# Optimization experiments

Measured on AMD Instinct MI355X. Metric: run time of the kernel, lower is better.

## Reference

```python
import jax, jax.numpy as jnp
import numpy as np

N_NODES = 100000


def gcn_layer(x, W, b, src, dst, n):
    # PyG GCNConv: h = x @ W; add self loops; norm = d^-1/2[src]*d^-1/2[dst];
    # out = scatter_add(norm * h[src] -> dst) + b
    h = x @ W  # [N, F_out]
    # append self loops
    loop = jnp.arange(n, dtype=src.dtype)
    s = jnp.concatenate([src, loop])
    d = jnp.concatenate([dst, loop])
    deg = jax.ops.segment_sum(jnp.ones_like(d, dtype=h.dtype), d, num_segments=n)
    dinv = jnp.where(deg > 0, jax.lax.rsqrt(deg), 0.0)
    norm = dinv[s] * dinv[d]  # [E+N]
    msg = h[s] * norm[:, None]  # gather + scale
    out = jax.ops.segment_sum(msg, d, num_segments=n)  # scatter-add
    return out + b


def setup_inputs() -> dict:
    key = jax.random.key(0)
    k1, k2, k3, k4 = jax.random.split(key, 4)
    din, dh = 64, 64
    x = jax.random.normal(k1, (N_NODES, din), dtype=jnp.float32)
    edge_index = jax.random.randint(k2, (2, 1600000), 0, N_NODES, dtype=jnp.int64)
    s1 = 1.0 / np.sqrt(din)
    s2 = 1.0 / np.sqrt(dh)
    W1 = jax.random.uniform(k3, (din, dh), dtype=jnp.float32, minval=-s1, maxval=s1)
    W2 = jax.random.uniform(k4, (dh, dh), dtype=jnp.float32, minval=-s2, maxval=s2)
    b1 = jnp.zeros((dh,), dtype=jnp.float32)
    b2 = jnp.zeros((dh,), dtype=jnp.float32)
    return {"x": x, "edge_index": edge_index, "W1": W1, "b1": b1, "W2": W2, "b2": b2}


def reference(x, edge_index, W1, b1, W2, b2):
    src, dst = edge_index[0], edge_index[1]
    n = x.shape[0]
    h = jax.nn.relu(gcn_layer(x, W1, b1, src, dst, n))
    h = jax.nn.relu(gcn_layer(h, W2, b2, src, dst, n))
    return h
```

## Files before the change

### kernel.cpp

```cpp
#include <hip/hip_runtime.h>
#include <hip/hip_bf16.h>

using bf16s = __hip_bfloat16;
typedef __bf16 bf16x8 __attribute__((ext_vector_type(8)));
typedef float f32x4 __attribute__((ext_vector_type(4)));

constexpr int MS_TILE = 4096;
constexpr int BSH = 8;
constexpr int BN = 256;
constexpr int NBUCK = 512;
constexpr int SLAB_CAP = 5120;
constexpr int CSR_CAP = 6912;

__device__ inline float uasf(unsigned u) { return __uint_as_float(u); }

__device__ inline unsigned pk2(float x, float y) {
    unsigned ux = __float_as_uint(x), uy = __float_as_uint(y);
    ux = (ux + 0x7fffu + ((ux >> 16) & 1u)) >> 16;
    uy = (uy + 0x7fffu + ((uy >> 16) & 1u)) & 0xffff0000u;
    return (ux & 0xffffu) | uy;
}

__global__ __launch_bounds__(256) void multisplit(const int* __restrict__ src,
                                                  const int* __restrict__ dst,
                                                  int* __restrict__ gcur,
                                                  int* __restrict__ part, int E) {
    __shared__ int cnt[NBUCK];
    __shared__ int off[NBUCK];
    __shared__ int gbase[NBUCK];
    __shared__ int img[MS_TILE];
    __shared__ int tgt[MS_TILE];
    int tid = threadIdx.x;
    int tbase = blockIdx.x * MS_TILE;
    int m = min(MS_TILE, E - tbase);
    for (int i = tid; i < NBUCK; i += 256) cnt[i] = 0;
    __syncthreads();
    int pk[16], bk[16], rk[16];
    int nloc = 0;
    int j0 = tid * 16;
    if (j0 + 16 <= m) {
#pragma unroll
        for (int h = 0; h < 4; h++) {
            int4 s4 = *(const int4*)(src + tbase + j0 + 4 * h);
            int4 d4 = *(const int4*)(dst + tbase + j0 + 4 * h);
            int ss[4] = {s4.x, s4.y, s4.z, s4.w};
            int dd[4] = {d4.x, d4.y, d4.z, d4.w};
#pragma unroll
            for (int k = 0; k < 4; k++) {
                int i = 4 * h + k;
                int b = dd[k] >> BSH;
                pk[i] = (ss[k] << BSH) | (dd[k] & (BN - 1));
                bk[i] = b;
                rk[i] = atomicAdd(&cnt[b], 1);
            }
        }
        nloc = 16;
    } else {
        for (int j = j0; j < m; j++) {
            int s = src[tbase + j], d = dst[tbase + j];
            int b = d >> BSH;
            pk[nloc] = (s << BSH) | (d & (BN - 1));
            bk[nloc] = b;
            rk[nloc] = atomicAdd(&cnt[b], 1);
            nloc++;
        }
    }
    __syncthreads();
    if (tid < 64) {
        int base = tid * 8;
        int vals[8];
        int s0 = 0;
#pragma unroll
        for (int j = 0; j < 8; j++) { vals[j] = cnt[base + j]; s0 += vals[j]; }
        int sc = s0;
#pragma unroll
        for (int o = 1; o < 64; o <<= 1) {
            int u = __shfl_up(sc, o);
            if (tid >= o) sc += u;
        }
        int ex = sc - s0;
#pragma unroll
        for (int j = 0; j < 8; j++) { off[base + j] = ex; ex += vals[j]; }
    }
    __syncthreads();
    for (int b = tid; b < NBUCK; b += 256) {
        int c = cnt[b];
        if (c) {
            int st = atomicAdd(&gcur[b], c);
            if (st > SLAB_CAP - c) st = SLAB_CAP - c;
            gbase[b] = b * SLAB_CAP + st;
        }
    }
    __syncthreads();
    for (int i = 0; i < nloc; i++) {
        int p = off[bk[i]] + rk[i];
        img[p] = pk[i];
        tgt[p] = gbase[bk[i]] + rk[i];
    }
    __syncthreads();
    for (int j = tid; j < m; j += 256) part[tgt[j]] = img[j];
}

__global__ __launch_bounds__(256) void bucket_place(const int* __restrict__ gcur,
                                                    const int* __restrict__ part,
                                                    int2* __restrict__ rinfo,
                                                    int* __restrict__ csr,
                                                    float* __restrict__ dinv, int n) {
    __shared__ int cnt[BN];
    __shared__ int cur[BN];
    __shared__ int wtot[4];
    __shared__ int img[CSR_CAP];
    int b = blockIdx.x;
    int tid = threadIdx.x;
    int node0 = b << BSH;
    int m = min(gcur[b], SLAB_CAP);
    const int* slab = part + b * SLAB_CAP;
    cnt[tid] = 0;
    __syncthreads();
    for (int j = tid; j < m; j += 256) atomicAdd(&cnt[slab[j] & (BN - 1)], 1);
    __syncthreads();
    int deg = cnt[tid];
    int pdeg = (deg + 7) & ~7;
    int lane = tid & 63, wv = tid >> 6;
    int sc = pdeg;
#pragma unroll
    for (int o = 1; o < 64; o <<= 1) {
        int u = __shfl_up(sc, o);
        if (lane >= o) sc += u;
    }
    if (lane == 63) wtot[wv] = sc;
    __syncthreads();
    int wbase = 0;
#pragma unroll
    for (int k = 0; k < 4; k++) wbase += (k < wv) ? wtot[k] : 0;
    int mpad = wtot[0] + wtot[1] + wtot[2] + wtot[3];
    int ex = sc - pdeg + wbase;
    cur[tid] = ex;
    int node = node0 + tid;
    if (node < n) {
        rinfo[node] = make_int2(b * CSR_CAP + ex, pdeg);
        dinv[node] = rsqrtf((float)(deg + 1));
    }
    int sent = n << 5;
    for (int j = ex + deg; j < ex + pdeg; j++) img[j] = sent;
    __syncthreads();
    for (int j = tid; j < m; j += 256) {
        int pkv = slab[j];
        int p = atomicAdd(&cur[pkv & (BN - 1)], 1);
        img[p] = (pkv >> BSH) << 5;
    }
    __syncthreads();
    int* dp = csr + b * CSR_CAP;
    for (int j = tid; j < mpad; j += 256) dp[j] = img[j];
}

template <bool AF32>
__global__ __launch_bounds__(256) void gemm64(const void* __restrict__ A_,
                                              const float* __restrict__ W,
                                              const float* __restrict__ dinv,
                                              bf16s* __restrict__ out, int nrows) {
    int lane = threadIdx.x & 63;
    int wid = (blockIdx.x * blockDim.x + threadIdx.x) >> 6;
    int nwaves = (gridDim.x * blockDim.x) >> 6;
    int r = lane & 15;
    int q = lane >> 4;
    int kb = q * 8;

    if (wid == 0) out[(size_t)nrows * 64 + lane] = __float2bfloat16(0.f);

    bf16x8 bfrag[4][2];
#pragma unroll
    for (int t = 0; t < 4; t++) {
#pragma unroll
        for (int h = 0; h < 2; h++) {
            bf16x8 bb;
            int ncol = t * 16 + r;
            int k0 = h * 32 + kb;
#pragma unroll
            for (int j = 0; j < 8; j++) bb[j] = (__bf16)W[(k0 + j) * 64 + ncol];
            bfrag[t][h] = bb;
        }
    }

    int ntiles = nrows >> 4;
    for (int tile = wid; tile < ntiles; tile += nwaves) {
        bf16x8 a0, a1;
        if (AF32) {
            const float* ap = (const float*)A_ + (size_t)(tile * 16 + r) * 64 + kb;
            f32x4 v0 = *reinterpret_cast<const f32x4*>(ap);
            f32x4 v1 = *reinterpret_cast<const f32x4*>(ap + 4);
            f32x4 v2 = *reinterpret_cast<const f32x4*>(ap + 32);
            f32x4 v3 = *reinterpret_cast<const f32x4*>(ap + 36);
#pragma unroll
            for (int j = 0; j < 4; j++) {
                a0[j] = (__bf16)v0[j]; a0[4 + j] = (__bf16)v1[j];
                a1[j] = (__bf16)v2[j]; a1[4 + j] = (__bf16)v3[j];
            }
        } else {
            const __bf16* ap = (const __bf16*)A_ + (size_t)(tile * 16 + r) * 64 + kb;
            a0 = *reinterpret_cast<const bf16x8*>(ap);
            a1 = *reinterpret_cast<const bf16x8*>(ap + 32);
        }
        f32x4 c[4];
#pragma unroll
        for (int t = 0; t < 4; t++) {
            f32x4 acc = {0.f, 0.f, 0.f, 0.f};
            acc = __builtin_amdgcn_mfma_f32_16x16x32_bf16(a0, bfrag[t][0], acc, 0, 0, 0);
            acc = __builtin_amdgcn_mfma_f32_16x16x32_bf16(a1, bfrag[t][1], acc, 0, 0, 0);
            c[t] = acc;
        }
        float dr[4];
#pragma unroll
        for (int g = 0; g < 4; g++) dr[g] = dinv[tile * 16 + q * 4 + g];
#pragma unroll
        for (int t = 0; t < 4; t++) {
#pragma unroll
            for (int g = 0; g < 4; g++) {
                int row = tile * 16 + q * 4 + g;
                out[(size_t)row * 64 + t * 16 + r] = __float2bfloat16(c[t][g] * dr[g]);
            }
        }
    }
}

template <bool OUTF32>
__global__ __launch_bounds__(256) void aggregate(const unsigned* __restrict__ t32,
                                                 const float* __restrict__ dinv,
                                                 const int2* __restrict__ rinfo,
                                                 const int* __restrict__ csr,
                                                 const float* __restrict__ bias,
                                                 void* __restrict__ out_, int n) {
    int gid = blockIdx.x * blockDim.x + threadIdx.x;
    int qw = gid >> 4;
    int v0 = qw * 2, v1 = v0 + 1;
    if (v0 >= n) return;
    bool has1 = v1 < n;
    int c = gid & 15;
    int2 r0 = rinfo[v0];
    int2 r1 = has1 ? rinfo[v1] : make_int2(0, 0);
    uint2 s0 = *(const uint2*)(t32 + (size_t)v0 * 32 + 2 * c);
    uint2 s1 = has1 ? *(const uint2*)(t32 + (size_t)v1 * 32 + 2 * c) : make_uint2(0, 0);
    float a00 = uasf(s0.x << 16), a01 = uasf(s0.x & 0xffff0000u);
    float a02 = uasf(s0.y << 16), a03 = uasf(s0.y & 0xffff0000u);
    float a10 = uasf(s1.x << 16), a11 = uasf(s1.x & 0xffff0000u);
    float a12 = uasf(s1.y << 16), a13 = uasf(s1.y & 0xffff0000u);
    const int* cp0 = csr + r0.x;
    const int* cp1 = csr + r1.x;
    int j0 = 0, j1 = 0;
    while (j0 < r0.y || j1 < r1.y) {
        bool g0 = j0 < r0.y, g1 = j1 < r1.y;
        int idx0[8], idx1[8];
        uint2 ga[8], gb[8];
        if (g0) {
            int4 e0 = *(const int4*)(cp0 + j0);
            int4 e1 = *(const int4*)(cp0 + j0 + 4);
            idx0[0]=e0.x; idx0[1]=e0.y; idx0[2]=e0.z; idx0[3]=e0.w;
            idx0[4]=e1.x; idx0[5]=e1.y; idx0[6]=e1.z; idx0[7]=e1.w;
#pragma unroll
            for (int k = 0; k < 8; k++)
                ga[k] = *(const uint2*)(t32 + (size_t)idx0[k] + 2 * c);
        }
        if (g1) {
            int4 e0 = *(const int4*)(cp1 + j1);
            int4 e1 = *(const int4*)(cp1 + j1 + 4);
            idx1[0]=e0.x; idx1[1]=e0.y; idx1[2]=e0.z; idx1[3]=e0.w;
            idx1[4]=e1.x; idx1[5]=e1.y; idx1[6]=e1.z; idx1[7]=e1.w;
#pragma unroll
            for (int k = 0; k < 8; k++)
                gb[k] = *(const uint2*)(t32 + (size_t)idx1[k] + 2 * c);
        }
        if (g0) {
#pragma unroll
            for (int k = 0; k < 8; k++) {
                a00 += uasf(ga[k].x << 16);
                a01 += uasf(ga[k].x & 0xffff0000u);
                a02 += uasf(ga[k].y << 16);
                a03 += uasf(ga[k].y & 0xffff0000u);
            }
            j0 += 8;
        }
        if (g1) {
#pragma unroll
            for (int k = 0; k < 8; k++) {
                a10 += uasf(gb[k].x << 16);
                a11 += uasf(gb[k].x & 0xffff0000u);
                a12 += uasf(gb[k].y << 16);
                a13 += uasf(gb[k].y & 0xffff0000u);
            }
            j1 += 8;
        }
    }
    f32x4 bb = ((const f32x4*)bias)[c];
    {
        float dv = dinv[v0];
        float o0 = fmaxf(fmaf(dv, a00, bb[0]), 0.f);
        float o1 = fmaxf(fmaf(dv, a01, bb[1]), 0.f);
        float o2 = fmaxf(fmaf(dv, a02, bb[2]), 0.f);
        float o3 = fmaxf(fmaf(dv, a03, bb[3]), 0.f);
        if (OUTF32) {
            f32x4 o4 = {o0, o1, o2, o3};
            ((f32x4*)out_)[(size_t)v0 * 16 + c] = o4;
        } else {
            uint2 ou; ou.x = pk2(o0, o1); ou.y = pk2(o2, o3);
            ((uint2*)out_)[(size_t)v0 * 16 + c] = ou;
        }
    }
    if (has1) {
        float dv = dinv[v1];
        float o0 = fmaxf(fmaf(dv, a10, bb[0]), 0.f);
        float o1 = fmaxf(fmaf(dv, a11, bb[1]), 0.f);
        float o2 = fmaxf(fmaf(dv, a12, bb[2]), 0.f);
        float o3 = fmaxf(fmaf(dv, a13, bb[3]), 0.f);
        if (OUTF32) {
            f32x4 o4 = {o0, o1, o2, o3};
            ((f32x4*)out_)[(size_t)v1 * 16 + c] = o4;
        } else {
            uint2 ou; ou.x = pk2(o0, o1); ou.y = pk2(o2, o3);
            ((uint2*)out_)[(size_t)v1 * 16 + c] = ou;
        }
    }
}

extern "C" void kernel_launch(void* const* d_in, const int* in_sizes, int n_in,
                              void* d_out, int out_size, void* d_ws, size_t ws_size,
                              hipStream_t stream) {
    const float* x  = (const float*)d_in[0];
    const int*   ei = (const int*)d_in[1];
    const float* W1 = (const float*)d_in[2];
    const float* b1 = (const float*)d_in[3];
    const float* W2 = (const float*)d_in[4];
    const float* b2 = (const float*)d_in[5];
    float* out = (float*)d_out;

    int n = in_sizes[0] / 64;
    int E = in_sizes[1] / 2;
    const int* src = ei;
    const int* dst = ei + E;
    int nbuck = (n + BN - 1) >> BSH;

    char* w = (char*)d_ws;
    auto alloc = [&](size_t bytes) -> void* {
        void* p = (void*)w;
        w += (bytes + 255) & ~(size_t)255;
        return p;
    };
    int*   gcur   = (int*)alloc(NBUCK * 4);
    int2*  rinfo  = (int2*)alloc((size_t)n * 8);
    int*   csr    = (int*)alloc((size_t)nbuck * CSR_CAP * 4);
    float* dinv   = (float*)alloc((size_t)n * 4);
    size_t slab_bytes = (size_t)nbuck * SLAB_CAP * 4;
    size_t tbuf_bytes = (size_t)(n + 16) * 64 * 2;
    char*  ovl    = (char*)alloc(slab_bytes > tbuf_bytes ? slab_bytes : tbuf_bytes);
    int*   part   = (int*)ovl;
    bf16s* tbuf   = (bf16s*)ovl;
    bf16s* h1     = (bf16s*)alloc((size_t)(n + 16) * 64 * 2);

    hipMemsetAsync(gcur, 0, NBUCK * 4, stream);

    int ntiles = (E + MS_TILE - 1) / MS_TILE;
    multisplit<<<ntiles, 256, 0, stream>>>(src, dst, gcur, part, E);
    bucket_place<<<nbuck, 256, 0, stream>>>(gcur, part, rinfo, csr, dinv, n);

    int agrid = (n * 8 + 255) / 256;
    gemm64<true><<<256, 256, 0, stream>>>(x, W1, dinv, tbuf, n);
    aggregate<false><<<agrid, 256, 0, stream>>>((const unsigned*)tbuf, dinv, rinfo, csr, b1, h1, n);
    gemm64<false><<<256, 256, 0, stream>>>(h1, W2, dinv, tbuf, n);
    aggregate<true><<<agrid, 256, 0, stream>>>((const unsigned*)tbuf, dinv, rinfo, csr, b2, out, n);
}
```

Before: 201.0 us.

## Scatter partition and CSR writes directly to global, drop LDS staging

The multisplit kernel no longer stages edges in shared memory with a bucket prefix scan before writing coalesced runs. Each thread now writes its packed edges straight to their global slab slot, and the tile shrinks to 2048 edges (8 per thread). The bucket_place kernel likewise writes sentinels and CSR entries straight to global instead of building an LDS image and copying it out. This removes a scan, several barriers and a large LDS footprint, which may raise occupancy, at the cost of scattered, uncoalesced global writes and more global atomics on the bucket counters.

```diff
diff --git a/kernel.cpp b/kernel.cpp
--- a/kernel.cpp
+++ b/kernel.cpp
@@ -5,7 +5,7 @@
 typedef __bf16 bf16x8 __attribute__((ext_vector_type(8)));
 typedef float f32x4 __attribute__((ext_vector_type(4)));
 
-constexpr int MS_TILE = 4096;
+constexpr int MS_TILE = 2048;
 constexpr int BSH = 8;
 constexpr int BN = 256;
 constexpr int NBUCK = 512;
@@ -26,35 +26,30 @@
                                                   int* __restrict__ gcur,
                                                   int* __restrict__ part, int E) {
     __shared__ int cnt[NBUCK];
-    __shared__ int off[NBUCK];
     __shared__ int gbase[NBUCK];
-    __shared__ int img[MS_TILE];
-    __shared__ int tgt[MS_TILE];
     int tid = threadIdx.x;
     int tbase = blockIdx.x * MS_TILE;
     int m = min(MS_TILE, E - tbase);
     for (int i = tid; i < NBUCK; i += 256) cnt[i] = 0;
     __syncthreads();
-    int pk[16], bk[16], rk[16];
+    int pk[8], bk[8], rk[8];
     int nloc = 0;
-    int j0 = tid * 16;
-    if (j0 + 16 <= m) {
-#pragma unroll
-        for (int h = 0; h < 4; h++) {
-            int4 s4 = *(const int4*)(src + tbase + j0 + 4 * h);
-            int4 d4 = *(const int4*)(dst + tbase + j0 + 4 * h);
-            int ss[4] = {s4.x, s4.y, s4.z, s4.w};
-            int dd[4] = {d4.x, d4.y, d4.z, d4.w};
-#pragma unroll
-            for (int k = 0; k < 4; k++) {
-                int i = 4 * h + k;
-                int b = dd[k] >> BSH;
-                pk[i] = (ss[k] << BSH) | (dd[k] & (BN - 1));
-                bk[i] = b;
-                rk[i] = atomicAdd(&cnt[b], 1);
-            }
-        }
-        nloc = 16;
+    int j0 = tid * 8;
+    if (j0 + 8 <= m) {
+        int4 s0 = *(const int4*)(src + tbase + j0);
+        int4 s1 = *(const int4*)(src + tbase + j0 + 4);
+        int4 d0 = *(const int4*)(dst + tbase + j0);
+        int4 d1 = *(const int4*)(dst + tbase + j0 + 4);
+        int ss[8] = {s0.x, s0.y, s0.z, s0.w, s1.x, s1.y, s1.z, s1.w};
+        int dd[8] = {d0.x, d0.y, d0.z, d0.w, d1.x, d1.y, d1.z, d1.w};
+#pragma unroll
+        for (int k = 0; k < 8; k++) {
+            int b = dd[k] >> BSH;
+            pk[k] = (ss[k] << BSH) | (dd[k] & (BN - 1));
+            bk[k] = b;
+            rk[k] = atomicAdd(&cnt[b], 1);
+        }
+        nloc = 8;
     } else {
         for (int j = j0; j < m; j++) {
             int s = src[tbase + j], d = dst[tbase + j];
@@ -66,23 +61,6 @@
         }
     }
     __syncthreads();
-    if (tid < 64) {
-        int base = tid * 8;
-        int vals[8];
-        int s0 = 0;
-#pragma unroll
-        for (int j = 0; j < 8; j++) { vals[j] = cnt[base + j]; s0 += vals[j]; }
-        int sc = s0;
-#pragma unroll
-        for (int o = 1; o < 64; o <<= 1) {
-            int u = __shfl_up(sc, o);
-            if (tid >= o) sc += u;
-        }
-        int ex = sc - s0;
-#pragma unroll
-        for (int j = 0; j < 8; j++) { off[base + j] = ex; ex += vals[j]; }
-    }
-    __syncthreads();
     for (int b = tid; b < NBUCK; b += 256) {
         int c = cnt[b];
         if (c) {
@@ -92,13 +70,9 @@
         }
     }
     __syncthreads();
-    for (int i = 0; i < nloc; i++) {
-        int p = off[bk[i]] + rk[i];
-        img[p] = pk[i];
-        tgt[p] = gbase[bk[i]] + rk[i];
-    }
-    __syncthreads();
-    for (int j = tid; j < m; j += 256) part[tgt[j]] = img[j];
+#pragma unroll
+    for (int i = 0; i < 8; i++)
+        if (i < nloc) part[gbase[bk[i]] + rk[i]] = pk[i];
 }
 
 __global__ __launch_bounds__(256) void bucket_place(const int* __restrict__ gcur,
@@ -109,7 +83,6 @@
     __shared__ int cnt[BN];
     __shared__ int cur[BN];
     __shared__ int wtot[4];
-    __shared__ int img[CSR_CAP];
     int b = blockIdx.x;
     int tid = threadIdx.x;
     int node0 = b << BSH;
@@ -133,7 +106,6 @@
     int wbase = 0;
 #pragma unroll
     for (int k = 0; k < 4; k++) wbase += (k < wv) ? wtot[k] : 0;
-    int mpad = wtot[0] + wtot[1] + wtot[2] + wtot[3];
     int ex = sc - pdeg + wbase;
     cur[tid] = ex;
     int node = node0 + tid;
@@ -141,17 +113,15 @@
         rinfo[node] = make_int2(b * CSR_CAP + ex, pdeg);
         dinv[node] = rsqrtf((float)(deg + 1));
     }
+    int* dp = csr + b * CSR_CAP;
     int sent = n << 5;
-    for (int j = ex + deg; j < ex + pdeg; j++) img[j] = sent;
+    for (int j = ex + deg; j < ex + pdeg; j++) dp[j] = sent;
     __syncthreads();
     for (int j = tid; j < m; j += 256) {
         int pkv = slab[j];
         int p = atomicAdd(&cur[pkv & (BN - 1)], 1);
-        img[p] = (pkv >> BSH) << 5;
-    }
-    __syncthreads();
-    int* dp = csr + b * CSR_CAP;
-    for (int j = tid; j < mpad; j += 256) dp[j] = img[j];
+        dp[p] = (pkv >> BSH) << 5;
+    }
 }
 
 template <bool AF32>
```

After: 219.4 us. 1.09x slower.
